# Optimization experiments

Measured on AMD Instinct MI355X. Metric: run time of the kernel, lower is better.

The kernel has to match this reference:

```python
import jax, jax.numpy as jnp
import numpy as np
from jax import lax

VOCAB, EMBED, HIDDEN, TAGS, SEQ = 50000, 300, 512, 12, 4096
START, STOP = 10, 11
NEG = -10000.0


def setup_inputs() -> dict:
    key = jax.random.key(0)
    ks = jax.random.split(key, 10)
    p = lambda k, shape: (jax.random.normal(k, shape, jnp.float32) * 0.1)
    transitions = jnp.zeros((TAGS, TAGS), jnp.float32)
    transitions = transitions.at[START, :].set(NEG).at[:, STOP].set(NEG)
    return {
        "sentence": jax.random.randint(ks[0], (SEQ,), 0, VOCAB),
        "embed_table": p(ks[1], (VOCAB, EMBED)),
        "Wih_f": p(ks[2], (4 * HIDDEN, EMBED)),
        "Whh_f": p(ks[3], (4 * HIDDEN, HIDDEN)),
        "bih_f": jnp.zeros((4 * HIDDEN,), jnp.float32),
        "bhh_f": jnp.zeros((4 * HIDDEN,), jnp.float32),
        "Wih_b": p(ks[4], (4 * HIDDEN, EMBED)),
        "Whh_b": p(ks[5], (4 * HIDDEN, HIDDEN)),
        "bih_b": jnp.zeros((4 * HIDDEN,), jnp.float32),
        "bhh_b": jnp.zeros((4 * HIDDEN,), jnp.float32),
        "W_out": p(ks[6], (TAGS, 2 * HIDDEN)),
        "b_out": jnp.zeros((TAGS,), jnp.float32),
        "transitions": transitions,
    }


def run_lstm(x, Wih, Whh, bih, bhh, reverse=False):
    # x: [T, E]; PyTorch gate order i, f, g, o
    H = Whh.shape[1]
    xg = x @ Wih.T + (bih + bhh)  # [T, 4H] precompute input projection

    def step(carry, g_in):
        h, c = carry
        g = g_in + h @ Whh.T
        i, f, gg, o = jnp.split(g, 4)
        i, f, o = jax.nn.sigmoid(i), jax.nn.sigmoid(f), jax.nn.sigmoid(o)
        c = f * c + i * jnp.tanh(gg)
        h = o * jnp.tanh(c)
        return (h, c), h

    init = (jnp.zeros((H,), x.dtype), jnp.zeros((H,), x.dtype))
    _, hs = lax.scan(step, init, xg, reverse=reverse)
    return hs  # [T, H], time-ordered


def lstm_features(sentence, embed_table, Wih_f, Whh_f, bih_f, bhh_f,
                  Wih_b, Whh_b, bih_b, bhh_b, W_out, b_out):
    emb = embed_table[sentence]  # [T, E]
    h_f = run_lstm(emb, Wih_f, Whh_f, bih_f, bhh_f, reverse=False)
    h_b = run_lstm(emb, Wih_b, Whh_b, bih_b, bhh_b, reverse=True)
    h = jnp.concatenate([h_f, h_b], axis=-1)  # [T, 2H]
    # dropout is identity in eval mode
    return h @ W_out.T + b_out  # [T, TAGS]


def viterbi(feats, transitions):
    K = feats.shape[1]
    init = jnp.full((K,), NEG, feats.dtype).at[START].set(0.0)

    def step(fv, feat):
        ntv = fv[None, :] + transitions  # [next, prev]
        bp = jnp.argmax(ntv, axis=1)
        return jnp.max(ntv, axis=1) + feat, bp

    fv, bps = lax.scan(step, init, feats)  # bps: [T, K]
    term = fv + transitions[STOP]
    term = term.at[STOP].set(NEG).at[START].set(NEG)
    best = jnp.argmax(term)
    score = term[best]

    def back(tag, bp):
        prev = bp[tag]
        return prev, prev

    _, chain = lax.scan(back, best, bps, reverse=True)  # chain[t] = tag at t-1
    path = jnp.concatenate([chain[1:], best[None]])  # [T] best tag sequence
    return score, path


def reference(sentence, embed_table, Wih_f, Whh_f, bih_f, bhh_f,
              Wih_b, Whh_b, bih_b, bhh_b, W_out, b_out, transitions):
    feats = lstm_features(sentence, embed_table, Wih_f, Whh_f, bih_f, bhh_f,
                          Wih_b, Whh_b, bih_b, bhh_b, W_out, b_out)
    score, path = viterbi(feats, transitions)
    return score, path
```

## Files before the change

### kernel.cpp

```cpp
#include <hip/hip_runtime.h>
#include <hip/hip_bf16.h>
#include <stdint.h>

#define SEQ_T 4096
#define EMB   300
#define HID   512
#define G4    2048
#define NTAG  12
#define TAG_START 10
#define TAG_STOP  11
#define NEGV  -10000.0f
#define NCHUNK 256
#define CLEN   16

#define OFF_XG    0
#define OFF_H     (OFF_XG + 2 * SEQ_T * G4)
#define OFF_HS    (OFF_H + 4096)
#define OFF_FEATS (OFF_HS + 2 * SEQ_T * HID)
#define OFF_VM    (OFF_FEATS + SEQ_T * NTAG)
#define OFF_VB    (OFF_VM + NCHUNK * 144)
#define OFF_VSC   (OFF_VB + NCHUNK * NTAG)
#define OFF_VP    (OFF_VSC + 8)
#define OFF_VMAP  (OFF_VP + NCHUNK * NTAG * 2)
#define WS_FLOATS (OFF_VMAP + NCHUNK * 2)

__device__ __forceinline__ float sigm_(float x) {
    return __fdividef(1.f, 1.f + __expf(-x));
}
__device__ __forceinline__ float tanh_(float x) {
    x = fminf(fmaxf(x, -15.f), 15.f);
    float e = __expf(2.f * x);
    return __fdividef(e - 1.f, e + 1.f);
}

__global__ __launch_bounds__(256) void k_xg(const int* __restrict__ sent,
                                            const float* __restrict__ table,
                                            const float* __restrict__ Wih_f,
                                            const float* __restrict__ bih_f,
                                            const float* __restrict__ bhh_f,
                                            const float* __restrict__ Wih_b,
                                            const float* __restrict__ bih_b,
                                            const float* __restrict__ bhh_b,
                                            float* __restrict__ ws) {
    __shared__ float As[64 * 105];
    __shared__ float Bs[64 * 105];
    __shared__ int rows[64];
    const int dir = blockIdx.z;
    const int g0  = blockIdx.x << 6;
    const int t0  = blockIdx.y << 6;
    const int tid = threadIdx.x;
    const float* __restrict__ Wih = dir ? Wih_b : Wih_f;
    const float* __restrict__ bih = dir ? bih_b : bih_f;
    const float* __restrict__ bhh = dir ? bhh_b : bhh_f;
    if (tid < 64) rows[tid] = sent[t0 + tid];
    __syncthreads();

    const int tg = (tid & 15) << 2;
    const int tp = (tid >> 4) << 2;
    float acc[4][4] = {{0.f}};

    for (int c = 0; c < 3; ++c) {
        const int k0 = c * 100;
        for (int e = tid; e < 64 * 100; e += 256) {
            int ti = e / 100, kk = e - ti * 100;
            As[ti * 105 + kk] = table[(size_t)rows[ti] * EMB + k0 + kk];
        }
        for (int e = tid; e < 64 * 100; e += 256) {
            int gi = e / 100, kk = e - gi * 100;
            Bs[gi * 105 + kk] = Wih[(size_t)(g0 + gi) * EMB + k0 + kk];
        }
        __syncthreads();
        for (int kk = 0; kk < 100; ++kk) {
            float a0 = As[(tp + 0) * 105 + kk];
            float a1 = As[(tp + 1) * 105 + kk];
            float a2 = As[(tp + 2) * 105 + kk];
            float a3 = As[(tp + 3) * 105 + kk];
            float b0 = Bs[(tg + 0) * 105 + kk];
            float b1 = Bs[(tg + 1) * 105 + kk];
            float b2 = Bs[(tg + 2) * 105 + kk];
            float b3 = Bs[(tg + 3) * 105 + kk];
            acc[0][0] = fmaf(a0, b0, acc[0][0]); acc[0][1] = fmaf(a0, b1, acc[0][1]);
            acc[0][2] = fmaf(a0, b2, acc[0][2]); acc[0][3] = fmaf(a0, b3, acc[0][3]);
            acc[1][0] = fmaf(a1, b0, acc[1][0]); acc[1][1] = fmaf(a1, b1, acc[1][1]);
            acc[1][2] = fmaf(a1, b2, acc[1][2]); acc[1][3] = fmaf(a1, b3, acc[1][3]);
            acc[2][0] = fmaf(a2, b0, acc[2][0]); acc[2][1] = fmaf(a2, b1, acc[2][1]);
            acc[2][2] = fmaf(a2, b2, acc[2][2]); acc[2][3] = fmaf(a2, b3, acc[2][3]);
            acc[3][0] = fmaf(a3, b0, acc[3][0]); acc[3][1] = fmaf(a3, b1, acc[3][1]);
            acc[3][2] = fmaf(a3, b2, acc[3][2]); acc[3][3] = fmaf(a3, b3, acc[3][3]);
        }
        __syncthreads();
    }
    float4 bv4 = *(const float4*)(bih + g0 + tg);
    float4 bh4 = *(const float4*)(bhh + g0 + tg);
    float4 bb = make_float4(bv4.x + bh4.x, bv4.y + bh4.y, bv4.z + bh4.z, bv4.w + bh4.w);
    #pragma unroll
    for (int i = 0; i < 4; ++i) {
        float4 r = make_float4(acc[i][0] + bb.x, acc[i][1] + bb.y,
                               acc[i][2] + bb.z, acc[i][3] + bb.w);
        *(float4*)(ws + OFF_XG + ((size_t)dir * SEQ_T + t0 + tp + i) * G4 + g0 + tg) = r;
    }
}

__global__ __launch_bounds__(512, 2) void k_scan(const float* __restrict__ Whh_f,
                                                 const float* __restrict__ Whh_b,
                                                 float* __restrict__ ws) {
    __shared__ float h_sh[2][8 * 68];
    const int bid = blockIdx.x;
    const int tid = threadIdx.x;
    const int dir = bid >> 5;
    const int wg  = bid & 31;
    const int wave = tid >> 6;
    const int lane = tid & 63;
    const int s  = lane >> 4;
    const int qq = (lane >> 3) & 1;
    const int p  = lane & 7;
    const int hu   = (wg << 4) + (wave << 1) + qq;
    const int gate = (s << 9) + hu;
    const float* __restrict__ Whh = dir ? Whh_b : Whh_f;

    float* xg = ws + OFF_XG + (size_t)dir * SEQ_T * G4;
    unsigned long long* hbuf = (unsigned long long*)(ws + OFF_H);
    float* hs = ws + OFF_HS + (size_t)dir * SEQ_T * HID;

    float4 w[16];
    {
        const float4* wrow = (const float4*)(Whh + (size_t)gate * HID + (p << 6));
        #pragma unroll
        for (int j = 0; j < 16; ++j) w[j] = wrow[j];
    }

    const bool owner = (s == 0) && (p == 0);
    float c = 0.f;
    float xg_cur = 0.f;
    if (p == 0) xg_cur = xg[(size_t)(dir ? (SEQ_T - 1) : 0) * G4 + gate];

    for (int k = 0; k < SEQ_T; ++k) {
        const int time = dir ? (SEQ_T - 1 - k) : k;
        float xg_nxt = 0.f;
        if (p == 0 && (k + 1) < SEQ_T)
            xg_nxt = xg[(size_t)(dir ? (time - 1) : (time + 1)) * G4 + gate];

        float acc = xg_cur;
        if (k > 0) {
            const unsigned want = (unsigned)(k - 1);
            unsigned long long* src = hbuf + ((size_t)(((k - 1) & 1) << 1) + dir) * HID;
            unsigned long long v;
            do {
                v = __hip_atomic_load(src + tid, __ATOMIC_RELAXED,
                                      __HIP_MEMORY_SCOPE_AGENT);
            } while ((unsigned)(v >> 32) != want);
            const int par = (k - 1) & 1;
            h_sh[par][wave * 68 + lane] = __uint_as_float((unsigned)v);
            __syncthreads();
            const float4* hp = (const float4*)(&h_sh[par][p * 68]);
            float ax = 0.f, ay = 0.f, az = 0.f, aw = 0.f;
            #pragma unroll
            for (int j = 0; j < 16; ++j) {
                float4 hv = hp[j];
                ax = fmaf(w[j].x, hv.x, ax);
                ay = fmaf(w[j].y, hv.y, ay);
                az = fmaf(w[j].z, hv.z, az);
                aw = fmaf(w[j].w, hv.w, aw);
            }
            acc += (ax + ay) + (az + aw);
        }
        acc += __shfl_xor(acc, 1);
        acc += __shfl_xor(acc, 2);
        acc += __shfl_xor(acc, 4);
        const int base = lane & 15;
        float gi = __shfl(acc, base + 0);
        float gf = __shfl(acc, base + 16);
        float gg = __shfl(acc, base + 32);
        float go = __shfl(acc, base + 48);
        if (owner) {
            float iv = sigm_(gi), fv = sigm_(gf), gv = tanh_(gg), ov = sigm_(go);
            c = fmaf(fv, c, iv * gv);
            float h = ov * tanh_(c);
            hs[(size_t)time * HID + hu] = h;
            unsigned long long pv = ((unsigned long long)(unsigned)k << 32) |
                                    (unsigned long long)__float_as_uint(h);
            __hip_atomic_store(&hbuf[((size_t)((k & 1) << 1) + dir) * HID + hu], pv,
                               __ATOMIC_RELAXED, __HIP_MEMORY_SCOPE_AGENT);
        }
        xg_cur = xg_nxt;
    }
}

__global__ __launch_bounds__(256) void k_feats(const float* __restrict__ Wout,
                                               const float* __restrict__ bout,
                                               float* __restrict__ ws) {
    const int t = blockIdx.x;
    const int tid = threadIdx.x;
    const float* hsf = ws + OFF_HS;
    const float* hsb = ws + OFF_HS + (size_t)SEQ_T * HID;
    float4 h4 = (tid < 128) ? ((const float4*)(hsf + (size_t)t * HID))[tid]
                            : ((const float4*)(hsb + (size_t)t * HID))[tid - 128];
    float pj[NTAG];
    #pragma unroll
    for (int j = 0; j < NTAG; ++j) {
        float4 wv = ((const float4*)(Wout + (size_t)j * 2 * HID))[tid];
        pj[j] = h4.x * wv.x + h4.y * wv.y + h4.z * wv.z + h4.w * wv.w;
    }
    #pragma unroll
    for (int j = 0; j < NTAG; ++j) {
        #pragma unroll
        for (int m = 1; m < 64; m <<= 1) pj[j] += __shfl_xor(pj[j], m);
    }
    __shared__ float red[4][NTAG];
    if ((tid & 63) == 0) {
        #pragma unroll
        for (int j = 0; j < NTAG; ++j) red[tid >> 6][j] = pj[j];
    }
    __syncthreads();
    if (tid < NTAG) {
        float v = red[0][tid] + red[1][tid] + red[2][tid] + red[3][tid] + bout[tid];
        ws[OFF_FEATS + (size_t)t * NTAG + tid] = v;
    }
}

__global__ __launch_bounds__(192) void k_vitA(const float* __restrict__ trans,
                                              float* __restrict__ ws) {
    __shared__ float M[NTAG][13];
    __shared__ float T[NTAG][NTAG];
    const int c = blockIdx.x;
    const int tid = threadIdx.x;
    const float* feats = ws + OFF_FEATS;
    const int j = tid / NTAG, i = tid - j * NTAG;
    if (tid < 144) T[j][i] = trans[tid];
    __syncthreads();
    float cur = 0.f;
    const int t0 = c * CLEN;
    if (tid < 144) cur = T[j][i] + feats[(size_t)t0 * NTAG + j];
    for (int t = t0 + 1; t < t0 + CLEN; ++t) {
        if (tid < 144) M[j][i] = cur;
        __syncthreads();
        if (tid < 144) {
            float fj = feats[(size_t)t * NTAG + j];
            float best = -3.4e38f;
            #pragma unroll
            for (int kk = 0; kk < NTAG; ++kk)
                best = fmaxf(best, T[j][kk] + M[kk][i]);
            cur = best + fj;
        }
        __syncthreads();
    }
    if (tid < 144) ws[OFF_VM + (size_t)c * 144 + tid] = cur;
}

__global__ __launch_bounds__(192) void k_vitB(const float* __restrict__ trans,
                                              float* __restrict__ ws,
                                              float* __restrict__ out) {
    __shared__ float Ms[NTAG][13];
    __shared__ float fvs[NTAG];
    const int tid = threadIdx.x;
    const int j = tid / NTAG, i = tid - j * NTAG;
    if (tid < NTAG) fvs[tid] = (tid == TAG_START) ? 0.f : NEGV;
    float m = (tid < 144) ? ws[OFF_VM + tid] : 0.f;
    for (int c = 0; c < NCHUNK; ++c) {
        if (tid < 144) Ms[j][i] = m;
        __syncthreads();
        if (tid < 144 && (c + 1) < NCHUNK)
            m = ws[OFF_VM + (size_t)(c + 1) * 144 + tid];
        float nf = 0.f;
        if (tid < NTAG) {
            ws[OFF_VB + (size_t)c * NTAG + tid] = fvs[tid];
            float best = -3.4e38f;
            #pragma unroll
            for (int kk = 0; kk < NTAG; ++kk)
                best = fmaxf(best, Ms[tid][kk] + fvs[kk]);
            nf = best;
        }
        __syncthreads();
        if (tid < NTAG) fvs[tid] = nf;
        __syncthreads();
    }
    if (tid == 0) {
        float bsc = -3.4e38f; int btag = 0;
        for (int q = 0; q < NTAG; ++q) {
            float tv = fvs[q] + trans[TAG_STOP * NTAG + q];
            if (q == TAG_START || q == TAG_STOP) tv = NEGV;
            if (tv > bsc) { bsc = tv; btag = q; }
        }
        out[0] = bsc;
        ((int*)(ws + OFF_VSC))[0] = btag;
    }
}

__global__ __launch_bounds__(256) void k_vitC(const float* __restrict__ trans,
                                              float* __restrict__ ws) {
    const int lane = threadIdx.x & 63;
    const int c = blockIdx.x * 4 + (threadIdx.x >> 6);
    const float* feats = ws + OFF_FEATS;
    float Trow[NTAG];
    #pragma unroll
    for (int i = 0; i < NTAG; ++i)
        Trow[i] = (lane < NTAG) ? trans[lane * NTAG + i] : -1e30f;
    float fv = (lane < NTAG) ? ws[OFF_VB + (size_t)c * NTAG + lane] : NEGV;

    unsigned bpLo[CLEN], bpHi[CLEN];
    const int t0 = c * CLEN;
    #pragma unroll
    for (int tt = 0; tt < CLEN; ++tt) {
        const int t = t0 + tt;
        float vv[NTAG];
        #pragma unroll
        for (int i = 0; i < NTAG; ++i) vv[i] = __shfl(fv, i) + Trow[i];
        float m0; int i0;
        {
            float a0 = vv[0];  int b0 = 0;  if (vv[1]  > a0) { a0 = vv[1];  b0 = 1; }
            float a1 = vv[2];  int b1 = 2;  if (vv[3]  > a1) { a1 = vv[3];  b1 = 3; }
            float a2 = vv[4];  int b2 = 4;  if (vv[5]  > a2) { a2 = vv[5];  b2 = 5; }
            float a3 = vv[6];  int b3 = 6;  if (vv[7]  > a3) { a3 = vv[7];  b3 = 7; }
            float a4 = vv[8];  int b4 = 8;  if (vv[9]  > a4) { a4 = vv[9];  b4 = 9; }
            float a5 = vv[10]; int b5 = 10; if (vv[11] > a5) { a5 = vv[11]; b5 = 11; }
            if (a1 > a0) { a0 = a1; b0 = b1; }
            if (a3 > a2) { a2 = a3; b2 = b3; }
            if (a5 > a4) { a4 = a5; b4 = b5; }
            if (a2 > a0) { a0 = a2; b0 = b2; }
            if (a4 > a0) { a0 = a4; b0 = b4; }
            m0 = a0; i0 = b0;
        }
        fv = (lane < NTAG) ? (m0 + feats[(size_t)t * NTAG + lane]) : NEGV;
        unsigned nib = (lane < NTAG) ? ((unsigned)i0 << ((lane & 7) << 2)) : 0u;
        nib |= __shfl_xor(nib, 1);
        nib |= __shfl_xor(nib, 2);
        nib |= __shfl_xor(nib, 4);
        bpLo[tt] = __shfl(nib, 0);
        bpHi[tt] = __shfl(nib, 8);
    }
    if (lane < NTAG) {
        int tag = lane;
        unsigned long long pk = 0ull;
        #pragma unroll
        for (int tt = CLEN - 1; tt >= 0; --tt) {
            pk |= ((unsigned long long)(unsigned)tag) << (tt << 2);
            unsigned wsel = (tag < 8) ? bpLo[tt] : bpHi[tt];
            tag = (int)((wsel >> ((tag & 7) << 2)) & 15u);
        }
        ((unsigned long long*)(ws + OFF_VP))[(size_t)c * NTAG + lane] = pk;
        unsigned long long mc = ((unsigned long long)(unsigned)tag) << (lane << 2);
        mc |= __shfl_xor(mc, 1);
        mc |= __shfl_xor(mc, 2);
        mc |= __shfl_xor(mc, 4);
        mc |= __shfl_xor(mc, 8);
        if (lane == 0) ((unsigned long long*)(ws + OFF_VMAP))[c] = mc;
    }
}

__global__ __launch_bounds__(64) void k_vitD(float* __restrict__ ws,
                                             float* __restrict__ out) {
    const int lane = threadIdx.x;
    const unsigned long long* vp = (const unsigned long long*)(ws + OFF_VP);
    const unsigned long long* vmap = (const unsigned long long*)(ws + OFF_VMAP);
    int tag = ((const int*)(ws + OFF_VSC))[0];
    for (int c = NCHUNK - 1; c >= 0; --c) {
        unsigned long long row = (lane < NTAG) ? vp[(size_t)c * NTAG + lane] : 0ull;
        unsigned long long mp = vmap[c];
        unsigned long long pk = __shfl(row, tag);
        if (lane < CLEN)
            out[c * CLEN + lane + 1] = (float)((pk >> (lane << 2)) & 15ull);
        tag = (int)((mp >> (tag << 2)) & 15ull);
    }
}

extern "C" void kernel_launch(void* const* d_in, const int* in_sizes, int n_in,
                              void* d_out, int out_size, void* d_ws, size_t ws_size,
                              hipStream_t stream) {
    const int*   sent  = (const int*)d_in[0];
    const float* table = (const float*)d_in[1];
    const float* Wih_f = (const float*)d_in[2];
    const float* Whh_f = (const float*)d_in[3];
    const float* bih_f = (const float*)d_in[4];
    const float* bhh_f = (const float*)d_in[5];
    const float* Wih_b = (const float*)d_in[6];
    const float* Whh_b = (const float*)d_in[7];
    const float* bih_b = (const float*)d_in[8];
    const float* bhh_b = (const float*)d_in[9];
    const float* Wout  = (const float*)d_in[10];
    const float* bout  = (const float*)d_in[11];
    const float* trans = (const float*)d_in[12];
    float* out = (float*)d_out;
    float* ws  = (float*)d_ws;
    if (ws_size < (size_t)WS_FLOATS * sizeof(float)) return;

    hipLaunchKernelGGL(k_xg, dim3(32, 64, 2), dim3(256), 0, stream, sent, table,
                       Wih_f, bih_f, bhh_f, Wih_b, bih_b, bhh_b, ws);
    hipLaunchKernelGGL(k_scan, dim3(64), dim3(512), 0, stream, Whh_f, Whh_b, ws);
    hipLaunchKernelGGL(k_feats, dim3(SEQ_T), dim3(256), 0, stream, Wout, bout, ws);
    hipLaunchKernelGGL(k_vitA, dim3(NCHUNK), dim3(192), 0, stream, trans, ws);
    hipLaunchKernelGGL(k_vitB, dim3(1), dim3(192), 0, stream, trans, ws, out);
    hipLaunchKernelGGL(k_vitC, dim3(NCHUNK / 4), dim3(256), 0, stream, trans, ws);
    hipLaunchKernelGGL(k_vitD, dim3(1), dim3(64), 0, stream, ws, out);
}
```

Before: 7.448 ms.

## Poll hidden state via sc0 loads with XCD-local placement and fallback buffer

The recurrent scan kernel now launches 256 blocks and keeps only those with bid&7 < 2, so all blocks of one direction should land on the same XCD under round-robin dispatch. Cross-block hidden-state exchange then uses sc0-scoped loads and stores, which the code relies on being coherent within an XCD's L2. A single wave polls 16 values per lane with wide vector loads instead of every thread spinning on an atomic. If the fast path has not seen the data after many tries, the kernel switches to a duplicate buffer written with agent-scope atomics, trading extra stores and reliance on dispatch placement for lower per-step synchronization latency.

```diff
diff --git a/kernel.cpp b/kernel.cpp
--- a/kernel.cpp
+++ b/kernel.cpp
@@ -15,7 +15,8 @@
 
 #define OFF_XG    0
 #define OFF_H     (OFF_XG + 2 * SEQ_T * G4)
-#define OFF_HS    (OFF_H + 4096)
+#define OFF_HB    (OFF_H + 4096)
+#define OFF_HS    (OFF_HB + 4096)
 #define OFF_FEATS (OFF_HS + 2 * SEQ_T * HID)
 #define OFF_VM    (OFF_FEATS + SEQ_T * NTAG)
 #define OFF_VB    (OFF_VM + NCHUNK * 144)
@@ -31,6 +32,36 @@
     x = fminf(fmaxf(x, -15.f), 15.f);
     float e = __expf(2.f * x);
     return __fdividef(e - 1.f, e + 1.f);
+}
+
+typedef unsigned int u32x4 __attribute__((ext_vector_type(4)));
+
+__device__ __forceinline__ void poll16_sc0(const unsigned long long* p,
+                                           u32x4& a, u32x4& b, u32x4& c, u32x4& d) {
+    asm volatile(
+        "global_load_dwordx4 %0, %4, off sc0\n\t"
+        "global_load_dwordx4 %1, %5, off sc0\n\t"
+        "global_load_dwordx4 %2, %6, off sc0\n\t"
+        "global_load_dwordx4 %3, %7, off sc0\n\t"
+        "s_waitcnt vmcnt(0)"
+        : "=&v"(a), "=&v"(b), "=&v"(c), "=&v"(d)
+        : "v"(p), "v"(p + 2), "v"(p + 4), "v"(p + 6)
+        : "memory");
+}
+__device__ __forceinline__ void poll16_sc1(const unsigned long long* p,
+                                           u32x4& a, u32x4& b, u32x4& c, u32x4& d) {
+    asm volatile(
+        "global_load_dwordx4 %0, %4, off sc0 sc1\n\t"
+        "global_load_dwordx4 %1, %5, off sc0 sc1\n\t"
+        "global_load_dwordx4 %2, %6, off sc0 sc1\n\t"
+        "global_load_dwordx4 %3, %7, off sc0 sc1\n\t"
+        "s_waitcnt vmcnt(0)"
+        : "=&v"(a), "=&v"(b), "=&v"(c), "=&v"(d)
+        : "v"(p), "v"(p + 2), "v"(p + 4), "v"(p + 6)
+        : "memory");
+}
+__device__ __forceinline__ void st_u64_sc0(unsigned long long* p, unsigned long long v) {
+    asm volatile("global_store_dwordx2 %0, %1, off sc0" :: "v"(p), "v"(v) : "memory");
 }
 
 __global__ __launch_bounds__(256) void k_xg(const int* __restrict__ sent,
@@ -106,9 +137,10 @@
                                                  float* __restrict__ ws) {
     __shared__ float h_sh[2][8 * 68];
     const int bid = blockIdx.x;
+    const int dir = bid & 7;
+    if (dir >= 2) return;
+    const int wg  = bid >> 3;
     const int tid = threadIdx.x;
-    const int dir = bid >> 5;
-    const int wg  = bid & 31;
     const int wave = tid >> 6;
     const int lane = tid & 63;
     const int s  = lane >> 4;
@@ -119,7 +151,8 @@
     const float* __restrict__ Whh = dir ? Whh_b : Whh_f;
 
     float* xg = ws + OFF_XG + (size_t)dir * SEQ_T * G4;
-    unsigned long long* hbuf = (unsigned long long*)(ws + OFF_H);
+    unsigned long long* bufA = (unsigned long long*)(ws + OFF_H);
+    unsigned long long* bufB = (unsigned long long*)(ws + OFF_HB);
     float* hs = ws + OFF_HS + (size_t)dir * SEQ_T * HID;
 
     float4 w[16];
@@ -133,6 +166,7 @@
     float c = 0.f;
     float xg_cur = 0.f;
     if (p == 0) xg_cur = xg[(size_t)(dir ? (SEQ_T - 1) : 0) * G4 + gate];
+    int slowmode = 0;
 
     for (int k = 0; k < SEQ_T; ++k) {
         const int time = dir ? (SEQ_T - 1 - k) : k;
@@ -142,15 +176,38 @@
 
         float acc = xg_cur;
         if (k > 0) {
-            const unsigned want = (unsigned)(k - 1);
-            unsigned long long* src = hbuf + ((size_t)(((k - 1) & 1) << 1) + dir) * HID;
-            unsigned long long v;
-            do {
-                v = __hip_atomic_load(src + tid, __ATOMIC_RELAXED,
-                                      __HIP_MEMORY_SCOPE_AGENT);
-            } while ((unsigned)(v >> 32) != want);
             const int par = (k - 1) & 1;
-            h_sh[par][wave * 68 + lane] = __uint_as_float((unsigned)v);
+            if (wave == 0) {
+                const unsigned want = (unsigned)k;
+                const size_t hb = ((size_t)(par << 1) + dir) * HID + ((size_t)lane << 3);
+                u32x4 q0, q1, q2, q3;
+                bool ok = false;
+                if (!slowmode) {
+                    int tries = 0;
+                    do {
+                        poll16_sc0(bufA + hb, q0, q1, q2, q3);
+                        ok = (q0[1] == want) & (q0[3] == want) &
+                             (q1[1] == want) & (q1[3] == want) &
+                             (q2[1] == want) & (q2[3] == want) &
+                             (q3[1] == want) & (q3[3] == want);
+                    } while (!ok && ++tries < 2048);
+                    if (!ok) slowmode = 1;
+                }
+                if (!ok) {
+                    do {
+                        poll16_sc1(bufB + hb, q0, q1, q2, q3);
+                        ok = (q0[1] == want) & (q0[3] == want) &
+                             (q1[1] == want) & (q1[3] == want) &
+                             (q2[1] == want) & (q2[3] == want) &
+                             (q3[1] == want) & (q3[3] == want);
+                    } while (!ok);
+                }
+                float* dst = &h_sh[par][((lane >> 3) * 68) + ((lane & 7) << 3)];
+                dst[0] = __uint_as_float(q0[0]); dst[1] = __uint_as_float(q0[2]);
+                dst[2] = __uint_as_float(q1[0]); dst[3] = __uint_as_float(q1[2]);
+                dst[4] = __uint_as_float(q2[0]); dst[5] = __uint_as_float(q2[2]);
+                dst[6] = __uint_as_float(q3[0]); dst[7] = __uint_as_float(q3[2]);
+            }
             __syncthreads();
             const float4* hp = (const float4*)(&h_sh[par][p * 68]);
             float ax = 0.f, ay = 0.f, az = 0.f, aw = 0.f;
@@ -177,9 +234,11 @@
             c = fmaf(fv, c, iv * gv);
             float h = ov * tanh_(c);
             hs[(size_t)time * HID + hu] = h;
-            unsigned long long pv = ((unsigned long long)(unsigned)k << 32) |
+            unsigned long long pv = ((unsigned long long)(unsigned)(k + 1) << 32) |
                                     (unsigned long long)__float_as_uint(h);
-            __hip_atomic_store(&hbuf[((size_t)((k & 1) << 1) + dir) * HID + hu], pv,
+            const size_t idx = ((size_t)((k & 1) << 1) + dir) * HID + hu;
+            st_u64_sc0(bufA + idx, pv);
+            __hip_atomic_store(&bufB[idx], pv,
                                __ATOMIC_RELAXED, __HIP_MEMORY_SCOPE_AGENT);
         }
         xg_cur = xg_nxt;
@@ -385,7 +444,7 @@
 
     hipLaunchKernelGGL(k_xg, dim3(32, 64, 2), dim3(256), 0, stream, sent, table,
                        Wih_f, bih_f, bhh_f, Wih_b, bih_b, bhh_b, ws);
-    hipLaunchKernelGGL(k_scan, dim3(64), dim3(512), 0, stream, Whh_f, Whh_b, ws);
+    hipLaunchKernelGGL(k_scan, dim3(256), dim3(512), 0, stream, Whh_f, Whh_b, ws);
     hipLaunchKernelGGL(k_feats, dim3(SEQ_T), dim3(256), 0, stream, Wout, bout, ws);
     hipLaunchKernelGGL(k_vitA, dim3(NCHUNK), dim3(192), 0, stream, trans, ws);
     hipLaunchKernelGGL(k_vitB, dim3(1), dim3(192), 0, stream, trans, ws, out);
```

New measurement: 13.43 ms. 1.8x slower.

## Pin each LSTM direction to one XCC and poll hidden state via L2 atomics

Applied to the files above, without the earlier changes.

Launches 256 scan blocks and keeps only those with blockIdx mod 8 in {0,1}, so that with round-robin XCC dispatch each direction's 32 workgroups land on the same XCD. Each block reads its XCC id and checks that all peers share it. If they do, the per-step hidden-state exchange uses L2-local atomic swap/or instructions instead of agent-scope loads and stores, cutting cross-die coherence latency in the serial recurrence. It also moves the step tags to k+1 and clears the exchange buffer in k_xg so stale values from a previous call cannot match. It relies on the dispatch-placement assumption and falls back to the old path otherwise.

```diff
diff --git a/kernel.cpp b/kernel.cpp
--- a/kernel.cpp
+++ b/kernel.cpp
@@ -22,7 +22,8 @@
 #define OFF_VSC   (OFF_VB + NCHUNK * NTAG)
 #define OFF_VP    (OFF_VSC + 8)
 #define OFF_VMAP  (OFF_VP + NCHUNK * NTAG * 2)
-#define WS_FLOATS (OFF_VMAP + NCHUNK * 2)
+#define OFF_XID   (OFF_VMAP + NCHUNK * 2)
+#define WS_FLOATS (OFF_XID + 64)
 
 __device__ __forceinline__ float sigm_(float x) {
     return __fdividef(1.f, 1.f + __expf(-x));
@@ -31,6 +32,17 @@
     x = fminf(fmaxf(x, -15.f), 15.f);
     float e = __expf(2.f * x);
     return __fdividef(e - 1.f, e + 1.f);
+}
+
+__device__ __forceinline__ void pub_l2(unsigned long long* p, unsigned long long v) {
+    asm volatile("global_atomic_swap_x2 %0, %1, off" :: "v"(p), "v"(v) : "memory");
+}
+__device__ __forceinline__ unsigned long long poll_l2(unsigned long long* p) {
+    unsigned long long old;
+    asm volatile("global_atomic_or_x2 %0, %1, %2, off sc0\n\t"
+                 "s_waitcnt vmcnt(0)"
+                 : "=v"(old) : "v"(p), "v"(0ULL) : "memory");
+    return old;
 }
 
 __global__ __launch_bounds__(256) void k_xg(const int* __restrict__ sent,
@@ -53,6 +65,11 @@
     const float* __restrict__ bih = dir ? bih_b : bih_f;
     const float* __restrict__ bhh = dir ? bhh_b : bhh_f;
     if (tid < 64) rows[tid] = sent[t0 + tid];
+    if (blockIdx.x == 0 && blockIdx.y == 0) {
+        for (int e = tid; e < 2048; e += 256)
+            ws[OFF_H + (size_t)blockIdx.z * 2048 + e] = 0.f;
+        if (blockIdx.z == 0 && tid < 64) ws[OFF_XID + tid] = 0.f;
+    }
     __syncthreads();
 
     const int tg = (tid & 15) << 2;
@@ -105,10 +122,12 @@
                                                  const float* __restrict__ Whh_b,
                                                  float* __restrict__ ws) {
     __shared__ float h_sh[2][8 * 68];
+    __shared__ int fastflag;
     const int bid = blockIdx.x;
+    const int dir = bid & 7;
+    if (dir >= 2) return;
+    const int wg  = bid >> 3;
     const int tid = threadIdx.x;
-    const int dir = bid >> 5;
-    const int wg  = bid & 31;
     const int wave = tid >> 6;
     const int lane = tid & 63;
     const int s  = lane >> 4;
@@ -129,6 +148,29 @@
         for (int j = 0; j < 16; ++j) w[j] = wrow[j];
     }
 
+    unsigned xcc;
+    asm volatile("s_getreg_b32 %0, hwreg(HW_REG_XCC_ID)" : "=s"(xcc));
+    xcc &= 0xffu;
+    {
+        unsigned* xid = (unsigned*)(ws + OFF_XID);
+        if (tid == 0)
+            __hip_atomic_store(&xid[dir * 32 + wg], xcc + 1u,
+                               __ATOMIC_RELAXED, __HIP_MEMORY_SCOPE_AGENT);
+        if (wave == 0) {
+            unsigned v = xcc + 1u;
+            if (lane < 32) {
+                do {
+                    v = __hip_atomic_load(&xid[dir * 32 + lane],
+                                          __ATOMIC_RELAXED, __HIP_MEMORY_SCOPE_AGENT);
+                } while (v == 0u);
+            }
+            unsigned long long b = __ballot(v == xcc + 1u);
+            if (lane == 0) fastflag = (b == ~0ull) ? 1 : 0;
+        }
+        __syncthreads();
+    }
+    const bool fast = (fastflag != 0);
+
     const bool owner = (s == 0) && (p == 0);
     float c = 0.f;
     float xg_cur = 0.f;
@@ -142,14 +184,18 @@
 
         float acc = xg_cur;
         if (k > 0) {
-            const unsigned want = (unsigned)(k - 1);
-            unsigned long long* src = hbuf + ((size_t)(((k - 1) & 1) << 1) + dir) * HID;
+            const unsigned want = (unsigned)k;
+            const int par = (k - 1) & 1;
+            unsigned long long* src = hbuf + ((size_t)(par << 1) + dir) * HID;
             unsigned long long v;
-            do {
-                v = __hip_atomic_load(src + tid, __ATOMIC_RELAXED,
-                                      __HIP_MEMORY_SCOPE_AGENT);
-            } while ((unsigned)(v >> 32) != want);
-            const int par = (k - 1) & 1;
+            if (fast) {
+                do { v = poll_l2(src + tid); } while ((unsigned)(v >> 32) != want);
+            } else {
+                do {
+                    v = __hip_atomic_load(src + tid, __ATOMIC_RELAXED,
+                                          __HIP_MEMORY_SCOPE_AGENT);
+                } while ((unsigned)(v >> 32) != want);
+            }
             h_sh[par][wave * 68 + lane] = __uint_as_float((unsigned)v);
             __syncthreads();
             const float4* hp = (const float4*)(&h_sh[par][p * 68]);
@@ -177,10 +223,12 @@
             c = fmaf(fv, c, iv * gv);
             float h = ov * tanh_(c);
             hs[(size_t)time * HID + hu] = h;
-            unsigned long long pv = ((unsigned long long)(unsigned)k << 32) |
+            unsigned long long pv = ((unsigned long long)(unsigned)(k + 1) << 32) |
                                     (unsigned long long)__float_as_uint(h);
-            __hip_atomic_store(&hbuf[((size_t)((k & 1) << 1) + dir) * HID + hu], pv,
-                               __ATOMIC_RELAXED, __HIP_MEMORY_SCOPE_AGENT);
+            unsigned long long* dst = &hbuf[((size_t)((k & 1) << 1) + dir) * HID + hu];
+            if (fast) pub_l2(dst, pv);
+            else __hip_atomic_store(dst, pv, __ATOMIC_RELAXED,
+                                    __HIP_MEMORY_SCOPE_AGENT);
         }
         xg_cur = xg_nxt;
     }
@@ -385,7 +433,7 @@
 
     hipLaunchKernelGGL(k_xg, dim3(32, 64, 2), dim3(256), 0, stream, sent, table,
                        Wih_f, bih_f, bhh_f, Wih_b, bih_b, bhh_b, ws);
-    hipLaunchKernelGGL(k_scan, dim3(64), dim3(512), 0, stream, Whh_f, Whh_b, ws);
+    hipLaunchKernelGGL(k_scan, dim3(256), dim3(512), 0, stream, Whh_f, Whh_b, ws);
     hipLaunchKernelGGL(k_feats, dim3(SEQ_T), dim3(256), 0, stream, Wout, bout, ws);
     hipLaunchKernelGGL(k_vitA, dim3(NCHUNK), dim3(192), 0, stream, trans, ws);
     hipLaunchKernelGGL(k_vitB, dim3(1), dim3(192), 0, stream, trans, ws, out);
```

Result: slower. 8.993 ms (+20.8%).

## Pipeline hidden-state polling with four in-flight uncached loads in inline asm

Applied to the files above, without the earlier changes.

Replaces the serial atomic-load spin loop in the recurrent scan with an inline-assembly poll that keeps four system-coherent loads in flight and exits when a value differs from the previously seen one. The tag now encodes k+1 and the h buffer is zeroed in the projection kernel, so change detection replaces equality-with-expected-step. The h store is moved before the hs write to publish sooner. This aims to cut inter-workgroup handoff latency per timestep, at the cost of fragile asm, reliance on value-change semantics, and extra memory traffic from polling.

```diff
diff --git a/kernel.cpp b/kernel.cpp
--- a/kernel.cpp
+++ b/kernel.cpp
@@ -32,6 +32,51 @@
     float e = __expf(2.f * x);
     return __fdividef(e - 1.f, e + 1.f);
 }
+
+#define POLL4(Q0, Q1, Q2, Q3, PREV, SRC, OUT) do {                          \
+    int idx_;                                                               \
+    asm volatile(                                                           \
+        "global_load_dwordx2 %[q0], %[a], off sc0 sc1\n\t"                 \
+        "global_load_dwordx2 %[q1], %[a], off sc0 sc1\n\t"                 \
+        "global_load_dwordx2 %[q2], %[a], off sc0 sc1\n\t"                 \
+        "global_load_dwordx2 %[q3], %[a], off sc0 sc1\n\t"                 \
+        "1:\n\t"                                                            \
+        "s_waitcnt vmcnt(3)\n\t"                                            \
+        "v_cmp_eq_u64 vcc, %[q0], %[pv]\n\t"                                \
+        "s_cbranch_vccz 2f\n\t"                                             \
+        "global_load_dwordx2 %[q0], %[a], off sc0 sc1\n\t"                 \
+        "s_waitcnt vmcnt(3)\n\t"                                            \
+        "v_cmp_eq_u64 vcc, %[q1], %[pv]\n\t"                                \
+        "s_cbranch_vccz 3f\n\t"                                             \
+        "global_load_dwordx2 %[q1], %[a], off sc0 sc1\n\t"                 \
+        "s_waitcnt vmcnt(3)\n\t"                                            \
+        "v_cmp_eq_u64 vcc, %[q2], %[pv]\n\t"                                \
+        "s_cbranch_vccz 4f\n\t"                                             \
+        "global_load_dwordx2 %[q2], %[a], off sc0 sc1\n\t"                 \
+        "s_waitcnt vmcnt(3)\n\t"                                            \
+        "v_cmp_eq_u64 vcc, %[q3], %[pv]\n\t"                                \
+        "s_cbranch_vccz 5f\n\t"                                             \
+        "global_load_dwordx2 %[q3], %[a], off sc0 sc1\n\t"                 \
+        "s_branch 1b\n\t"                                                   \
+        "2:\n\t"                                                            \
+        "s_mov_b32 %[i], 0\n\t"                                             \
+        "s_branch 6f\n\t"                                                   \
+        "3:\n\t"                                                            \
+        "s_mov_b32 %[i], 1\n\t"                                             \
+        "s_branch 6f\n\t"                                                   \
+        "4:\n\t"                                                            \
+        "s_mov_b32 %[i], 2\n\t"                                             \
+        "s_branch 6f\n\t"                                                   \
+        "5:\n\t"                                                            \
+        "s_mov_b32 %[i], 3\n\t"                                             \
+        "6:\n\t"                                                            \
+        : [q0] "+v"(Q0), [q1] "+v"(Q1), [q2] "+v"(Q2), [q3] "+v"(Q3),      \
+          [i] "=s"(idx_)                                                    \
+        : [a] "v"(SRC), [pv] "v"(PREV)                                      \
+        : "vcc", "memory");                                                 \
+    OUT = (idx_ == 0) ? Q0 : (idx_ == 1) ? Q1 : (idx_ == 2) ? Q2 : Q3;     \
+    PREV = OUT;                                                             \
+} while (0)
 
 __global__ __launch_bounds__(256) void k_xg(const int* __restrict__ sent,
                                             const float* __restrict__ table,
@@ -53,6 +98,10 @@
     const float* __restrict__ bih = dir ? bih_b : bih_f;
     const float* __restrict__ bhh = dir ? bhh_b : bhh_f;
     if (tid < 64) rows[tid] = sent[t0 + tid];
+    if (blockIdx.x == 0 && blockIdx.y == 0) {
+        for (int e = tid; e < 2048; e += 256)
+            ws[OFF_H + (size_t)blockIdx.z * 2048 + e] = 0.f;
+    }
     __syncthreads();
 
     const int tg = (tid & 15) << 2;
@@ -106,9 +155,9 @@
                                                  float* __restrict__ ws) {
     __shared__ float h_sh[2][8 * 68];
     const int bid = blockIdx.x;
-    const int tid = threadIdx.x;
     const int dir = bid >> 5;
     const int wg  = bid & 31;
+    const int tid = threadIdx.x;
     const int wave = tid >> 6;
     const int lane = tid & 63;
     const int s  = lane >> 4;
@@ -134,6 +183,10 @@
     float xg_cur = 0.f;
     if (p == 0) xg_cur = xg[(size_t)(dir ? (SEQ_T - 1) : 0) * G4 + gate];
 
+    unsigned long long pa0 = 0, pa1 = 0, pa2 = 0, pa3 = 0;
+    unsigned long long pb0 = 0, pb1 = 0, pb2 = 0, pb3 = 0;
+    unsigned long long prevA = 0, prevB = 0;
+
     for (int k = 0; k < SEQ_T; ++k) {
         const int time = dir ? (SEQ_T - 1 - k) : k;
         float xg_nxt = 0.f;
@@ -142,14 +195,14 @@
 
         float acc = xg_cur;
         if (k > 0) {
-            const unsigned want = (unsigned)(k - 1);
-            unsigned long long* src = hbuf + ((size_t)(((k - 1) & 1) << 1) + dir) * HID;
+            const int par = (k - 1) & 1;
+            unsigned long long* src = hbuf + ((size_t)(par << 1) + dir) * HID + tid;
             unsigned long long v;
-            do {
-                v = __hip_atomic_load(src + tid, __ATOMIC_RELAXED,
-                                      __HIP_MEMORY_SCOPE_AGENT);
-            } while ((unsigned)(v >> 32) != want);
-            const int par = (k - 1) & 1;
+            if (par == 0) {
+                POLL4(pa0, pa1, pa2, pa3, prevA, src, v);
+            } else {
+                POLL4(pb0, pb1, pb2, pb3, prevB, src, v);
+            }
             h_sh[par][wave * 68 + lane] = __uint_as_float((unsigned)v);
             __syncthreads();
             const float4* hp = (const float4*)(&h_sh[par][p * 68]);
@@ -176,14 +229,15 @@
             float iv = sigm_(gi), fv = sigm_(gf), gv = tanh_(gg), ov = sigm_(go);
             c = fmaf(fv, c, iv * gv);
             float h = ov * tanh_(c);
-            hs[(size_t)time * HID + hu] = h;
-            unsigned long long pv = ((unsigned long long)(unsigned)k << 32) |
+            unsigned long long pv = ((unsigned long long)(unsigned)(k + 1) << 32) |
                                     (unsigned long long)__float_as_uint(h);
             __hip_atomic_store(&hbuf[((size_t)((k & 1) << 1) + dir) * HID + hu], pv,
                                __ATOMIC_RELAXED, __HIP_MEMORY_SCOPE_AGENT);
+            hs[(size_t)time * HID + hu] = h;
         }
         xg_cur = xg_nxt;
     }
+    asm volatile("s_waitcnt vmcnt(0)" ::: "memory");
 }
 
 __global__ __launch_bounds__(256) void k_feats(const float* __restrict__ Wout,
```

Result: slower. 7.700 ms (+3.4%).
